# Kernel tuning notes

Measured on AMD Instinct MI355X. Metric: run time of the kernel, lower is better.

The kernel has to match this reference:

```python
import jax, jax.numpy as jnp
import numpy as np

B, T, H, NIN, NOUT = 16, 64, 256, 2, 2
ALPHA = 0.25       # alpha_time_scale
BETA = 0.1         # beta_time_scale
SIGMA_SYN = 0.002
PERT_SIGMA = 0.1   # neural-noise sigma used only at t == perturbed_time


def setup_inputs() -> dict:
    key = jax.random.key(0)
    ks = jax.random.split(key, 8)
    return {
        'input_signal': jax.random.normal(ks[0], (B, T, NIN), jnp.float32),
        'hidden': jax.random.normal(ks[1], (B, H), jnp.float32) * 0.1,
        'w_in': jax.random.normal(ks[2], (H, NIN), jnp.float32) / np.sqrt(NIN).astype(np.float32),
        'w_hh': jax.random.normal(ks[3], (H, H), jnp.float32) / np.sqrt(H).astype(np.float32),
        'b_hh': jnp.zeros((H,), jnp.float32),
        'w_out': jax.random.normal(ks[4], (NOUT, H), jnp.float32) / np.sqrt(H).astype(np.float32),
        'noise_pert': jax.random.normal(ks[5], (B, H), jnp.float32),
        'syn_noise': jax.random.normal(ks[6], (T, B, H, H), jnp.float32),
        'perturbed_time': 32,
    }


def reference(input_signal, hidden, w_in, w_hh, b_hh, w_out, noise_pert, syn_noise, perturbed_time):
    # input_signal: [B,T,NIN]; hidden: [B,H]; plasticity (beta != 0) + anti-Hebbian branch.
    dt = input_signal.dtype
    Bn, Tn, _ = input_signal.shape
    Hn = hidden.shape[1]
    alpha = jnp.full((Hn,), ALPHA, dt)            # broadcasts over last (hidden) axis
    beta = jnp.full((Hn,), BETA, dt)
    sqrt_alpha = jnp.sqrt(alpha)
    sqrt_beta = jnp.sqrt(beta)

    xs_in = jnp.moveaxis(input_signal, 1, 0)      # [T,B,NIN]
    # new_j starts at w_hh; different_j = new_j - w_hh == 0, so it is derived each step.
    new_j0 = jnp.broadcast_to(w_hh, (Bn, Hn, Hn)).astype(dt)

    def step(carry, xs):
        h, new_j = carry
        x_t, sn_t, t = xs
        act = jnp.tanh(h)                                      # [B,H]
        diff_j = new_j - w_hh                                  # [B,H,H]
        # torch.matmul(act.unsqueeze(1), different_j).squeeze(1)
        dj_act = jnp.einsum('bi,bij->bj', act, diff_j)
        tmp = x_t @ w_in.T + act @ w_hh.T + b_hh + dj_act      # [B,H]
        noise = jnp.where(t == perturbed_time,
                          noise_pert * PERT_SIGMA * sqrt_alpha,
                          jnp.zeros((), dt))
        h = (1.0 - alpha) * h + alpha * tmp + noise
        # anti-Hebbian: -outer(act, act) + randn * sigma_syn * sqrt(beta)
        add_w = -jnp.einsum('bi,bj->bij', act, act) + sn_t * SIGMA_SYN * sqrt_beta
        new_j = new_j + beta * add_w                           # beta broadcasts on last axis
        out = h @ w_out.T                                      # [B,NOUT]
        return (h, new_j), (h, out)

    (h_fin, new_j), (hid_list, out_list) = jax.lax.scan(
        step, (hidden, new_j0), (xs_in, syn_noise, jnp.arange(Tn)))
    # [T,B,*] -> [B,T,*], matching the final permute in torch
    return (jnp.moveaxis(hid_list, 0, 1), jnp.moveaxis(out_list, 0, 1), h_fin, new_j)
```

## Files before the change

kernel.cpp:

```cpp
#include <hip/hip_runtime.h>

#define BB 16
#define TT 64
#define HH 256
#define NSUB 16
#define NBLK (BB * NSUB)

#define OUT_OFF  (BB * TT * HH)
#define HFIN_OFF (OUT_OFF + BB * TT * 2)
#define NJ_OFF   (HFIN_OFF + BB * HH)

#define C_SN    6.324555320336759e-05f
#define C_NOISE 0.05f

typedef unsigned long long u64;
typedef unsigned int u32;

__device__ __forceinline__ void slot_put(u64* p, u64 v) {
    (void)__hip_atomic_exchange(p, v, __ATOMIC_RELAXED, __HIP_MEMORY_SCOPE_AGENT);
}
__device__ __forceinline__ u64 slot_get(u64* p) {
    return __hip_atomic_fetch_add(p, 0ull, __ATOMIC_RELAXED, __HIP_MEMORY_SCOPE_AGENT);
}
__device__ __forceinline__ u64 pack(u32 tag, float v) {
    return ((u64)tag << 32) | (u64)__float_as_uint(v);
}

#define LGKM_BAR() do {                                          \
    asm volatile("s_waitcnt lgkmcnt(0)" ::: "memory");           \
    __builtin_amdgcn_sched_barrier(0);                           \
    __builtin_amdgcn_s_barrier();                                \
    __builtin_amdgcn_sched_barrier(0);                           \
} while (0)

#define STEP(T, CUR, NXT, BF, BI)                                            \
{                                                                            \
    const u32 tagw = (u32)((T) + 1);                                         \
    if ((T) > 0) {                                                           \
        _Pragma("unroll")                                                    \
        for (int m = 0; m < 16; ++m) M[m] += C_SN * BF[m];                   \
    }                                                                        \
    {                                                                        \
        const float* snp = sn + (((size_t)(T) * BB + b) * HH + rbase) * HH + jcol; \
        _Pragma("unroll")                                                    \
        for (int m = 0; m < 16; ++m) BI[m] = snp[(size_t)(16 * m) * HH];     \
    }                                                                        \
               \
    float a[16];                                                             \
    _Pragma("unroll")                                                        \
    for (int mq = 0; mq < 4; ++mq) {                                         \
        float4 v = *(const float4*)&s_actT[CUR][rbase * 16 + mq * 4];        \
        a[mq * 4 + 0] = v.x; a[mq * 4 + 1] = v.y;                            \
        a[mq * 4 + 2] = v.z; a[mq * 4 + 3] = v.w;                            \
    }                                                                        \
    float p = 0.f;                                                           \
    _Pragma("unroll")                                                        \
    for (int m = 0; m < 16; ++m) p += a[m] * M[m];                           \
    p += __shfl_xor(p, 16, 64);                                              \
    p += __shfl_xor(p, 32, 64);                                              \
    if (ln < 16) s_red[wv][ln] = p;                                          \
    LGKM_BAR();                                         \
    if (tid < 16) {                                                          \
        const float dj = s_red[0][tid] + s_red[1][tid]                       \
                       + s_red[2][tid] + s_red[3][tid];                      \
        const float tmp = s_x[2 * (T)] * wi0 + s_x[2 * (T) + 1] * wi1        \
                        + bh + dj;                                           \
        hreg = 0.75f * hreg + 0.25f * tmp + (((T) == pt) ? npv : 0.f);       \
        slot_put(slotb + ((CUR) * NSUB + sub) * 16 + tid, pack(tagw, hreg)); \
        s_h[NXT][jcol] = hreg;                                               \
        s_actT[NXT][q * 16 + sub] = tanhf(hreg);                             \
        dout[((size_t)b * TT + (T)) * HH + jcol] = hreg;                     \
    }                                                                        \
            \
    {                                                                        \
        const float aj = s_actT[CUR][q * 16 + sub];                          \
        _Pragma("unroll")                                                    \
        for (int m = 0; m < 16; ++m) M[m] -= 0.1f * a[m] * aj;               \
    }                                                                        \
    if (sub == 1) {                                                          \
        const float hv = s_h[CUR][tid];                                      \
        float p0 = hv * wo0, p1 = hv * wo1;                                  \
        _Pragma("unroll")                                                    \
        for (int off = 32; off; off >>= 1) {                                 \
            p0 += __shfl_down(p0, off, 64);                                  \
            p1 += __shfl_down(p1, off, 64);                                  \
        }                                                                    \
        if (ln == 0) { s_o[wv][0] = p0; s_o[wv][1] = p1; }                   \
    }                                                                        \
            \
    if (tid < 240) {                                                         \
        int fs = tid >> 4; fs += (fs >= sub);                                \
        const int fq = tid & 15;                                             \
        u64* sp = slotb + ((CUR) * NSUB + fs) * 16 + fq;                     \
        u64 v = slot_get(sp);                                                \
        while ((u32)(v >> 32) != tagw) {                                     \
            __builtin_amdgcn_s_sleep(1);                                     \
            v = slot_get(sp);                                                \
        }                                                                    \
        const float hr = __uint_as_float((u32)v);                            \
        s_h[NXT][fs * 16 + fq] = hr;                                         \
        s_actT[NXT][fq * 16 + fs] = tanhf(hr);                               \
    }                                                                        \
    LGKM_BAR();                                         \
    if (sub == 1 && tid == 0 && (T) > 0) {                                   \
        dout[OUT_OFF + ((size_t)b * TT + ((T) - 1)) * 2 + 0] =               \
            s_o[0][0] + s_o[1][0] + s_o[2][0] + s_o[3][0];                   \
        dout[OUT_OFF + ((size_t)b * TT + ((T) - 1)) * 2 + 1] =               \
            s_o[0][1] + s_o[1][1] + s_o[2][1] + s_o[3][1];                   \
    }                                                                        \
}

__global__ __launch_bounds__(256) void rnn_all(
    const float* __restrict__ x,
    const float* __restrict__ h0,
    const float* __restrict__ w_in,
    const float* __restrict__ w_hh,
    const float* __restrict__ b_hh,
    const float* __restrict__ w_out,
    const float* __restrict__ nper,
    const float* __restrict__ sn,
    const int*   __restrict__ pt_ptr,
    float*       __restrict__ dout,
    u64*         __restrict__ ws)
{
    const int tid = threadIdx.x;
    const int bid = blockIdx.x;
    const int b   = bid >> 4;
    const int sub = bid & 15;
    const int j0  = sub * 16;
    const int q     = tid & 15;
    const int rbase = tid >> 4;
    const int jcol  = j0 + q;
    const int wv = tid >> 6, ln = tid & 63;

    __shared__ float s_actT[2][HH];
    __shared__ float s_h[2][HH];
    __shared__ float s_red[4][16];
    __shared__ float s_o[4][2];
    __shared__ float s_x[2 * TT];
    __shared__ float s_wt[16][HH];

    u64* slotb = ws + (size_t)b * (2 * NSUB * 16);
    const int pt = *pt_ptr;

    for (int idx = tid; idx < 16 * HH; idx += 256)
        s_wt[idx >> 8][idx & 255] = w_hh[(size_t)(j0 + (idx >> 8)) * HH + (idx & 255)];
    {
        const float hv = h0[b * HH + tid];
        s_h[0][tid] = hv;
        s_actT[0][(tid & 15) * 16 + (tid >> 4)] = tanhf(hv);
    }
    if (tid < 2 * TT) s_x[tid] = x[b * 2 * TT + tid];

    float wi0 = 0.f, wi1 = 0.f, bh = 0.f, npv = 0.f, hreg = 0.f;
    if (tid < 16) {
        wi0  = w_in[jcol * 2 + 0];
        wi1  = w_in[jcol * 2 + 1];
        bh   = b_hh[jcol];
        npv  = nper[b * HH + jcol] * C_NOISE;
        hreg = h0[b * HH + jcol];
    }
    const float wo0 = w_out[tid], wo1 = w_out[HH + tid];
    __syncthreads();

    float M[16];
    #pragma unroll
    for (int m = 0; m < 16; ++m) M[m] = s_wt[q][rbase + 16 * m];

    float bufA[16], bufB[16];

    for (int tt = 0; tt < TT; tt += 2) {
        STEP(tt,     0, 1, bufB, bufA)
        STEP(tt + 1, 1, 0, bufA, bufB)
    }

    #pragma unroll
    for (int m = 0; m < 16; ++m) M[m] += C_SN * bufB[m];

    if (sub == 1) {
        const float hv = s_h[0][tid];
        float p0 = hv * wo0, p1 = hv * wo1;
        #pragma unroll
        for (int off = 32; off; off >>= 1) {
            p0 += __shfl_down(p0, off, 64);
            p1 += __shfl_down(p1, off, 64);
        }
        if (ln == 0) { s_o[wv][0] = p0; s_o[wv][1] = p1; }
        __syncthreads();
        if (tid == 0) {
            dout[OUT_OFF + ((size_t)b * TT + (TT - 1)) * 2 + 0] =
                s_o[0][0] + s_o[1][0] + s_o[2][0] + s_o[3][0];
            dout[OUT_OFF + ((size_t)b * TT + (TT - 1)) * 2 + 1] =
                s_o[0][1] + s_o[1][1] + s_o[2][1] + s_o[3][1];
        }
    }
    if (sub == 2) dout[HFIN_OFF + b * HH + tid] = s_h[0][tid];

    #pragma unroll
    for (int m = 0; m < 16; ++m) {
        const int i = rbase + 16 * m;
        dout[NJ_OFF + ((size_t)b * HH + i) * HH + jcol] =
            w_hh[(size_t)i * HH + jcol] + M[m] - s_wt[q][i];
    }
}

extern "C" void kernel_launch(void* const* d_in, const int* in_sizes, int n_in,
                              void* d_out, int out_size, void* d_ws, size_t ws_size,
                              hipStream_t stream) {
    (void)in_sizes; (void)n_in; (void)out_size; (void)ws_size;
    const float* x     = (const float*)d_in[0];
    const float* h0    = (const float*)d_in[1];
    const float* w_in  = (const float*)d_in[2];
    const float* w_hh  = (const float*)d_in[3];
    const float* b_hh  = (const float*)d_in[4];
    const float* w_out = (const float*)d_in[5];
    const float* nper  = (const float*)d_in[6];
    const float* sn    = (const float*)d_in[7];
    const int*   pt    = (const int*)d_in[8];
    float* dout        = (float*)d_out;
    u64* ws            = (u64*)d_ws;

    hipMemsetAsync(d_ws, 0, (size_t)BB * 2 * NSUB * 16 * sizeof(u64), stream);

    rnn_all<<<dim3(NBLK), dim3(256), 0, stream>>>(
        x, h0, w_in, w_hh, b_hh, w_out, nper, sn, pt, dout, ws);
}
```

Before: 135.8 us.

## Remap threads so each wave owns four columns and reduces via shuffles

Each wave now owns four output columns and each lane four rows, held in a 4x4 register tile. The matrix-vector partials are fully reduced with xor shuffles inside the wave, so the shared-memory reduction and one block barrier per timestep are gone. The noise and weight loads become float4 reads, and the cross-block slot layout is flattened per column. In exchange, each lane now reads 16-byte pieces from different rows of the large noise tensor, so coalescing across a wave is worse. The wave-level reduction also needs more shuffle rounds.

Result: slower. 159.5 us (+17.5%).

```diff
diff --git a/kernel.cpp b/kernel.cpp
--- a/kernel.cpp
+++ b/kernel.cpp
@@ -36,72 +36,93 @@
 #define STEP(T, CUR, NXT, BF, BI)                                            \
 {                                                                            \
     const u32 tagw = (u32)((T) + 1);                                         \
+    \
     if ((T) > 0) {                                                           \
         _Pragma("unroll")                                                    \
-        for (int m = 0; m < 16; ++m) M[m] += C_SN * BF[m];                   \
-    }                                                                        \
-    {                                                                        \
-        const float* snp = sn + (((size_t)(T) * BB + b) * HH + rbase) * HH + jcol; \
-        _Pragma("unroll")                                                    \
-        for (int m = 0; m < 16; ++m) BI[m] = snp[(size_t)(16 * m) * HH];     \
-    }                                                                        \
-               \
-    float a[16];                                                             \
+        for (int c = 0; c < 4; ++c)                                          \
+            _Pragma("unroll")                                                \
+            for (int r = 0; r < 4; ++r) M[c][r] += C_SN * BF[r][c];          \
+    }                                                                        \
+                             \
+    {                                                                        \
+        const float* snp = sn + (((size_t)(T) * BB + b) * HH + 4 * l) * HH + C0; \
+        _Pragma("unroll")                                                    \
+        for (int r = 0; r < 4; ++r) {                                        \
+            float4 v = *(const float4*)&snp[(size_t)r * HH];                 \
+            BI[r][0] = v.x; BI[r][1] = v.y; BI[r][2] = v.z; BI[r][3] = v.w;  \
+        }                                                                    \
+    }                                                                        \
+     \
+    float a[4];                                                              \
+    {                                                                        \
+        float4 av = *(const float4*)&s_act[CUR][4 * l];                      \
+        a[0] = av.x; a[1] = av.y; a[2] = av.z; a[3] = av.w;                  \
+    }                                                                        \
+    float p0 = 0.f, p1 = 0.f, p2 = 0.f, p3 = 0.f;                            \
     _Pragma("unroll")                                                        \
-    for (int mq = 0; mq < 4; ++mq) {                                         \
-        float4 v = *(const float4*)&s_actT[CUR][rbase * 16 + mq * 4];        \
-        a[mq * 4 + 0] = v.x; a[mq * 4 + 1] = v.y;                            \
-        a[mq * 4 + 2] = v.z; a[mq * 4 + 3] = v.w;                            \
-    }                                                                        \
-    float p = 0.f;                                                           \
+    for (int r = 0; r < 4; ++r) {                                            \
+        p0 += a[r] * M[0][r]; p1 += a[r] * M[1][r];                          \
+        p2 += a[r] * M[2][r]; p3 += a[r] * M[3][r];                          \
+    }                                                                        \
+             \
     _Pragma("unroll")                                                        \
-    for (int m = 0; m < 16; ++m) p += a[m] * M[m];                           \
-    p += __shfl_xor(p, 16, 64);                                              \
-    p += __shfl_xor(p, 32, 64);                                              \
-    if (ln < 16) s_red[wv][ln] = p;                                          \
-    LGKM_BAR();                                         \
-    if (tid < 16) {                                                          \
-        const float dj = s_red[0][tid] + s_red[1][tid]                       \
-                       + s_red[2][tid] + s_red[3][tid];                      \
-        const float tmp = s_x[2 * (T)] * wi0 + s_x[2 * (T) + 1] * wi1        \
-                        + bh + dj;                                           \
-        hreg = 0.75f * hreg + 0.25f * tmp + (((T) == pt) ? npv : 0.f);       \
-        slot_put(slotb + ((CUR) * NSUB + sub) * 16 + tid, pack(tagw, hreg)); \
-        s_h[NXT][jcol] = hreg;                                               \
-        s_actT[NXT][q * 16 + sub] = tanhf(hreg);                             \
-        dout[((size_t)b * TT + (T)) * HH + jcol] = hreg;                     \
-    }                                                                        \
-            \
-    {                                                                        \
-        const float aj = s_actT[CUR][q * 16 + sub];                          \
-        _Pragma("unroll")                                                    \
-        for (int m = 0; m < 16; ++m) M[m] -= 0.1f * a[m] * aj;               \
-    }                                                                        \
+    for (int off = 1; off < 64; off <<= 1) {                                 \
+        p0 += __shfl_xor(p0, off, 64); p1 += __shfl_xor(p1, off, 64);        \
+        p2 += __shfl_xor(p2, off, 64); p3 += __shfl_xor(p3, off, 64);        \
+    }                                                                        \
+             \
+    {                                                                        \
+        const float x0 = s_x[2 * (T)], x1 = s_x[2 * (T) + 1];                \
+        const float pf = ((T) == pt) ? 1.f : 0.f;                            \
+        hc[0] = 0.75f * hc[0] + 0.25f * (x0 * wi0c[0] + x1 * wi1c[0] + bhc[0] + p0) + pf * npvc[0]; \
+        hc[1] = 0.75f * hc[1] + 0.25f * (x0 * wi0c[1] + x1 * wi1c[1] + bhc[1] + p1) + pf * npvc[1]; \
+        hc[2] = 0.75f * hc[2] + 0.25f * (x0 * wi0c[2] + x1 * wi1c[2] + bhc[2] + p2) + pf * npvc[2]; \
+        hc[3] = 0.75f * hc[3] + 0.25f * (x0 * wi0c[3] + x1 * wi1c[3] + bhc[3] + p3) + pf * npvc[3]; \
+    }                                                                        \
+         \
+    if (l < 4) {                                                             \
+        const float hv = (l == 0) ? hc[0] : (l == 1) ? hc[1]                 \
+                       : (l == 2) ? hc[2] : hc[3];                           \
+        slot_put(slotb + (CUR) * HH + (C0 + l), pack(tagw, hv));             \
+        s_h[NXT][C0 + l] = hv;                                               \
+        s_act[NXT][C0 + l] = tanhf(hv);                                      \
+        dout[((size_t)b * TT + (T)) * HH + C0 + l] = hv;                     \
+    }                                                                        \
+                              \
+    {                                                                        \
+        float4 acv = *(const float4*)&s_act[CUR][C0];                        \
+        float ac[4] = { acv.x, acv.y, acv.z, acv.w };                        \
+        _Pragma("unroll")                                                    \
+        for (int c = 0; c < 4; ++c)                                          \
+            _Pragma("unroll")                                                \
+            for (int r = 0; r < 4; ++r) M[c][r] -= 0.1f * a[r] * ac[c];      \
+    }                                                                        \
+                          \
     if (sub == 1) {                                                          \
         const float hv = s_h[CUR][tid];                                      \
-        float p0 = hv * wo0, p1 = hv * wo1;                                  \
+        float q0 = hv * wo0, q1 = hv * wo1;                                  \
         _Pragma("unroll")                                                    \
         for (int off = 32; off; off >>= 1) {                                 \
-            p0 += __shfl_down(p0, off, 64);                                  \
-            p1 += __shfl_down(p1, off, 64);                                  \
+            q0 += __shfl_down(q0, off, 64);                                  \
+            q1 += __shfl_down(q1, off, 64);                                  \
         }                                                                    \
-        if (ln == 0) { s_o[wv][0] = p0; s_o[wv][1] = p1; }                   \
+        if (l == 0) { s_o[wv][0] = q0; s_o[wv][1] = q1; }                    \
     }                                                                        \
             \
     if (tid < 240) {                                                         \
         int fs = tid >> 4; fs += (fs >= sub);                                \
-        const int fq = tid & 15;                                             \
-        u64* sp = slotb + ((CUR) * NSUB + fs) * 16 + fq;                     \
+        const int fcol = fs * 16 + (tid & 15);                               \
+        u64* sp = slotb + (CUR) * HH + fcol;                                 \
         u64 v = slot_get(sp);                                                \
         while ((u32)(v >> 32) != tagw) {                                     \
             __builtin_amdgcn_s_sleep(1);                                     \
             v = slot_get(sp);                                                \
         }                                                                    \
         const float hr = __uint_as_float((u32)v);                            \
-        s_h[NXT][fs * 16 + fq] = hr;                                         \
-        s_actT[NXT][fq * 16 + fs] = tanhf(hr);                               \
-    }                                                                        \
-    LGKM_BAR();                                         \
+        s_h[NXT][fcol] = hr;                                                 \
+        s_act[NXT][fcol] = tanhf(hr);                                        \
+    }                                                                        \
+    LGKM_BAR();                                 \
     if (sub == 1 && tid == 0 && (T) > 0) {                                   \
         dout[OUT_OFF + ((size_t)b * TT + ((T) - 1)) * 2 + 0] =               \
             s_o[0][0] + s_o[1][0] + s_o[2][0] + s_o[3][0];                   \
@@ -127,47 +148,49 @@
     const int bid = blockIdx.x;
     const int b   = bid >> 4;
     const int sub = bid & 15;
-    const int j0  = sub * 16;
-    const int q     = tid & 15;
-    const int rbase = tid >> 4;
-    const int jcol  = j0 + q;
-    const int wv = tid >> 6, ln = tid & 63;
-
-    __shared__ float s_actT[2][HH];
+    const int wv  = tid >> 6;
+    const int l   = tid & 63;
+    const int C0  = sub * 16 + wv * 4;
+
+    __shared__ float s_act[2][HH];
     __shared__ float s_h[2][HH];
-    __shared__ float s_red[4][16];
     __shared__ float s_o[4][2];
     __shared__ float s_x[2 * TT];
-    __shared__ float s_wt[16][HH];
-
-    u64* slotb = ws + (size_t)b * (2 * NSUB * 16);
+
+    u64* slotb = ws + (size_t)b * (2 * HH);
     const int pt = *pt_ptr;
 
-    for (int idx = tid; idx < 16 * HH; idx += 256)
-        s_wt[idx >> 8][idx & 255] = w_hh[(size_t)(j0 + (idx >> 8)) * HH + (idx & 255)];
     {
         const float hv = h0[b * HH + tid];
         s_h[0][tid] = hv;
-        s_actT[0][(tid & 15) * 16 + (tid >> 4)] = tanhf(hv);
+        s_act[0][tid] = tanhf(hv);
     }
     if (tid < 2 * TT) s_x[tid] = x[b * 2 * TT + tid];
 
-    float wi0 = 0.f, wi1 = 0.f, bh = 0.f, npv = 0.f, hreg = 0.f;
-    if (tid < 16) {
-        wi0  = w_in[jcol * 2 + 0];
-        wi1  = w_in[jcol * 2 + 1];
-        bh   = b_hh[jcol];
-        npv  = nper[b * HH + jcol] * C_NOISE;
-        hreg = h0[b * HH + jcol];
+    float wi0c[4], wi1c[4], bhc[4], npvc[4], hc[4];
+    #pragma unroll
+    for (int c = 0; c < 4; ++c) {
+        wi0c[c] = w_in[(C0 + c) * 2 + 0];
+        wi1c[c] = w_in[(C0 + c) * 2 + 1];
+        bhc[c]  = b_hh[C0 + c];
+        npvc[c] = nper[b * HH + C0 + c] * C_NOISE;
+    }
+    {
+        float4 hv = *(const float4*)&h0[b * HH + C0];
+        hc[0] = hv.x; hc[1] = hv.y; hc[2] = hv.z; hc[3] = hv.w;
     }
     const float wo0 = w_out[tid], wo1 = w_out[HH + tid];
+
+    float M[4][4], Mi[4][4];
+    #pragma unroll
+    for (int c = 0; c < 4; ++c) {
+        float4 v = *(const float4*)&w_hh[(size_t)(C0 + c) * HH + 4 * l];
+        M[c][0] = v.x; M[c][1] = v.y; M[c][2] = v.z; M[c][3] = v.w;
+        Mi[c][0] = v.x; Mi[c][1] = v.y; Mi[c][2] = v.z; Mi[c][3] = v.w;
+    }
+
+    float bufA[4][4], bufB[4][4];
     __syncthreads();
-
-    float M[16];
-    #pragma unroll
-    for (int m = 0; m < 16; ++m) M[m] = s_wt[q][rbase + 16 * m];
-
-    float bufA[16], bufB[16];
 
     for (int tt = 0; tt < TT; tt += 2) {
         STEP(tt,     0, 1, bufB, bufA)
@@ -175,17 +198,19 @@
     }
 
     #pragma unroll
-    for (int m = 0; m < 16; ++m) M[m] += C_SN * bufB[m];
+    for (int c = 0; c < 4; ++c)
+        #pragma unroll
+        for (int r = 0; r < 4; ++r) M[c][r] += C_SN * bufB[r][c];
 
     if (sub == 1) {
         const float hv = s_h[0][tid];
-        float p0 = hv * wo0, p1 = hv * wo1;
+        float q0 = hv * wo0, q1 = hv * wo1;
         #pragma unroll
         for (int off = 32; off; off >>= 1) {
-            p0 += __shfl_down(p0, off, 64);
-            p1 += __shfl_down(p1, off, 64);
+            q0 += __shfl_down(q0, off, 64);
+            q1 += __shfl_down(q1, off, 64);
         }
-        if (ln == 0) { s_o[wv][0] = p0; s_o[wv][1] = p1; }
+        if (l == 0) { s_o[wv][0] = q0; s_o[wv][1] = q1; }
         __syncthreads();
         if (tid == 0) {
             dout[OUT_OFF + ((size_t)b * TT + (TT - 1)) * 2 + 0] =
@@ -197,10 +222,15 @@
     if (sub == 2) dout[HFIN_OFF + b * HH + tid] = s_h[0][tid];
 
     #pragma unroll
-    for (int m = 0; m < 16; ++m) {
-        const int i = rbase + 16 * m;
-        dout[NJ_OFF + ((size_t)b * HH + i) * HH + jcol] =
-            w_hh[(size_t)i * HH + jcol] + M[m] - s_wt[q][i];
+    for (int r = 0; r < 4; ++r) {
+        const int i = 4 * l + r;
+        float4 wrow = *(const float4*)&w_hh[(size_t)i * HH + C0];
+        float4 o;
+        o.x = wrow.x + M[0][r] - Mi[0][r];
+        o.y = wrow.y + M[1][r] - Mi[1][r];
+        o.z = wrow.z + M[2][r] - Mi[2][r];
+        o.w = wrow.w + M[3][r] - Mi[3][r];
+        *(float4*)&dout[NJ_OFF + ((size_t)b * HH + i) * HH + C0] = o;
     }
 }
 
@@ -220,7 +250,7 @@
     float* dout        = (float*)d_out;
     u64* ws            = (u64*)d_ws;
 
-    hipMemsetAsync(d_ws, 0, (size_t)BB * 2 * NSUB * 16 * sizeof(u64), stream);
+    hipMemsetAsync(d_ws, 0, (size_t)BB * 2 * HH * sizeof(u64), stream);
 
     rnn_all<<<dim3(NBLK), dim3(256), 0, stream>>>(
         x, h0, w_in, w_hh, b_hh, w_out, nper, sn, pt, dout, ws);
```
